# Kernel tuning notes

Hardware: AMD Instinct MI355X
Metric: run time of the kernel (lower is better)

## Reference

```python
import jax, jax.numpy as jnp
import numpy as np

B, N, D, H = 2, 2048, 1024, 16
DH = D // H            # 64
PH = 3 * DH            # 192 per-head proj dim (module quirk: 3*Dh per head)
P = H * PH             # 3072 total projection width


def setup_inputs() -> dict:
    key = jax.random.key(0)
    ks = jax.random.split(key, 8)
    s = 0.02
    return {
        "input": jax.random.normal(ks[0], (B, N, D), dtype=jnp.float32),
        "q_w": jax.random.normal(ks[1], (D, P), dtype=jnp.float32) * s,
        "q_b": jnp.zeros((P,), dtype=jnp.float32),
        "k_w": jax.random.normal(ks[2], (D, P), dtype=jnp.float32) * s,
        "k_b": jnp.zeros((P,), dtype=jnp.float32),
        "v_w": jax.random.normal(ks[3], (D, P), dtype=jnp.float32) * s,
        "v_b": jnp.zeros((P,), dtype=jnp.float32),
        "o_w": jax.random.normal(ks[4], (P, D), dtype=jnp.float32) * s,
        "o_b": jnp.zeros((D,), dtype=jnp.float32),
    }


def reference(input, q_w, q_b, k_w, k_b, v_w, v_b, o_w, o_b):
    def heads(y):  # [B,N,H*PH] -> [B,H,N,PH]
        return y.reshape(B, N, H, PH).transpose(0, 2, 1, 3)

    q_mat = heads(input @ q_w + q_b)
    # faithful to source: v_mat uses the 'k' projection, k_mat uses the 'v' projection
    v_mat = heads(input @ k_w + k_b)
    k_mat = heads(input @ v_w + v_b)

    scale = 1.0 / jnp.sqrt(jnp.float32(DH * H))  # sqrt(dim), per source
    scores = jnp.einsum('bhnd,bhmd->bhnm', q_mat, k_mat) * scale
    weights = jax.nn.softmax(scores, axis=-1)
    inter = jnp.einsum('bhnm,bhmd->bhnd', weights, v_mat)
    inter = inter.transpose(0, 2, 1, 3).reshape(B, N, P)  # b n (h d)
    return inter @ o_w + o_b
```

## Files before the change

kernel.cpp:

```cpp
#include <hip/hip_runtime.h>
#include <cstdint>
#include <cstddef>

typedef __bf16 bf16;
typedef __attribute__((ext_vector_type(8))) __bf16 bf16x8;
typedef __attribute__((ext_vector_type(4))) __bf16 bf16x4;
typedef __attribute__((ext_vector_type(2))) __bf16 bf16x2;
typedef __attribute__((ext_vector_type(4))) float f32x4;

#define MFMA_16x16x32(a, b, c) __builtin_amdgcn_mfma_f32_16x16x32_bf16((a), (b), (c), 0, 0, 0)

__device__ __forceinline__ void gload_lds16(const void* g, void* l) {
  __builtin_amdgcn_global_load_lds((__attribute__((address_space(1))) void*)g,
                                   (__attribute__((address_space(3))) void*)l,
                                   16, 0, 0);
}

__global__ __launch_bounds__(256) void cvt_x_kernel(const float* __restrict__ in,
                                                    bf16* __restrict__ out) {
  int i = blockIdx.x * 256 + threadIdx.x;
  float4 v = ((const float4*)in)[i];
  bf16x4 o = {(bf16)v.x, (bf16)v.y, (bf16)v.z, (bf16)v.w};
  ((bf16x4*)out)[i] = o;
}

__global__ __launch_bounds__(256) void transpose_cvt_kernel(const float* __restrict__ in,
                                                            bf16* __restrict__ out,
                                                            int R, int C) {
  __shared__ float tile[32][33];
  int tiles_c = C >> 5;
  int br = (int)blockIdx.x / tiles_c, bc = (int)blockIdx.x % tiles_c;
  int r0 = br << 5, c0 = bc << 5;
  int tr = threadIdx.x >> 5, tc = threadIdx.x & 31;
#pragma unroll
  for (int i = 0; i < 4; i++)
    tile[tr + 8 * i][tc] = in[(size_t)(r0 + tr + 8 * i) * C + c0 + tc];
  __syncthreads();
#pragma unroll
  for (int i = 0; i < 4; i++) {
    int oc = tr + 8 * i;
    out[(size_t)(c0 + oc) * R + r0 + tc] = (bf16)tile[tc][oc];
  }
}

__global__ __launch_bounds__(512, 2) void gemm_fused_qkv(
    const bf16* __restrict__ A, const bf16* __restrict__ Bt,
    const float* __restrict__ q_b, const float* __restrict__ v_b,
    const float* __restrict__ k_b,
    bf16* __restrict__ Qm, bf16* __restrict__ Km, bf16* __restrict__ Vt) {
  constexpr int K = 1024, NT = 16;
  __shared__ __align__(16) bf16 sA[2][2][128 * 32];
  __shared__ __align__(16) bf16 sB[2][192 * 64];

  int bid = blockIdx.x;
  int xcd = bid & 7, j = bid >> 3;
  int bm = xcd * 4 + (j & 3), bn = j >> 2;
  int m0 = bm << 7, n0 = bn * 192;

  int tid = threadIdx.x, lane = tid & 63, w = tid >> 6;
  int wr = w >> 2, wc = w & 3;
  int l15 = lane & 15, lg = lane >> 4;

  int sra = lane >> 2, sca = lane & 3;
  const bf16* gA = A + (size_t)(m0 + w * 16 + sra) * K + ((sca ^ ((sra >> 1) & 3)) * 8);
  int srb = lane >> 3, scb = lane & 7;
  const bf16* gB = Bt + (size_t)(n0 + w * 24 + srb) * K + ((scb ^ srb) * 8);

#define STAGE_AB(BUF, T)                                                   \
  {                                                                        \
    _Pragma("unroll") for (int kh = 0; kh < 2; kh++)                       \
        gload_lds16(gA + (size_t)(T) * 64 + kh * 32, &sA[BUF][kh][w * 512]); \
    _Pragma("unroll") for (int ii = 0; ii < 3; ii++)                       \
        gload_lds16(gB + (size_t)(ii * 8) * K + (T) * 64,                  \
                    &sB[BUF][(w * 3 + ii) * 512]);                         \
  }
#define VMCNT(N) asm volatile("s_waitcnt vmcnt(" #N ")" ::: "memory")
#define LGK0                                           \
  {                                                    \
    asm volatile("s_waitcnt lgkmcnt(0)" ::: "memory"); \
    __builtin_amdgcn_sched_barrier(0);                 \
  }

  int slotA = lg ^ ((l15 >> 1) & 3);
  int aBase = wr * 2048 + l15 * 32 + slotA * 8;
  int bBase = (wc * 48 + l15) * 64;
  int sB0 = (lg ^ (l15 & 7)) * 8;
  int sB1 = ((4 + lg) ^ (l15 & 7)) * 8;

#define RD_A(BUF, KH)                                                      \
  _Pragma("unroll") for (int mf = 0; mf < 4; mf++)                         \
      a[mf] = *(const bf16x8*)&sA[BUF][KH][aBase + mf * 512];
#define RD_B(BUF, SLOT)                                                    \
  _Pragma("unroll") for (int nf = 0; nf < 3; nf++)                         \
      b[nf] = *(const bf16x8*)&sB[BUF][bBase + nf * 1024 + (SLOT)];
#define MFMA12                                                             \
  _Pragma("unroll") for (int mf = 0; mf < 4; mf++)                         \
      _Pragma("unroll") for (int nf = 0; nf < 3; nf++)                     \
          acc[mf][nf] = MFMA_16x16x32(a[mf], b[nf], acc[mf][nf]);

  f32x4 acc[4][3];
#pragma unroll
  for (int mf = 0; mf < 4; mf++)
#pragma unroll
    for (int nf = 0; nf < 3; nf++) acc[mf][nf] = (f32x4){0.f, 0.f, 0.f, 0.f};

  STAGE_AB(0, 0);

#pragma unroll 2
  for (int s = 0; s < NT; s++) {
    int buf = s & 1, nbuf = buf ^ 1;
    int nxt = (s + 1) & (NT - 1);
    bf16x8 a[4], b[3];

    STAGE_AB(nbuf, nxt);
    VMCNT(5);
    __builtin_amdgcn_s_barrier();

    RD_A(buf, 0);
    RD_B(buf, sB0);
    LGK0;
    __builtin_amdgcn_s_setprio(1);
    MFMA12;
    __builtin_amdgcn_s_setprio(0);

    RD_A(buf, 1);
    RD_B(buf, sB1);
    LGK0;
    __builtin_amdgcn_s_barrier();
    __builtin_amdgcn_s_setprio(1);
    MFMA12;
    __builtin_amdgcn_s_setprio(0);
  }

  int seg = bn >> 4;
  int segbn = bn & 15;
  const float* bias = seg == 0 ? q_b : (seg == 1 ? v_b : k_b);
  bf16* outQK = seg == 0 ? Qm : Km;
#pragma unroll
  for (int mf = 0; mf < 4; mf++) {
#pragma unroll
    for (int nf = 0; nf < 3; nf++) {
      int colL = segbn * 192 + wc * 48 + nf * 16 + l15;
      int row0 = m0 + wr * 64 + mf * 16 + lg * 4;
      float bv = bias[colL];
      if (seg < 2) {
#pragma unroll
        for (int r = 0; r < 4; r++)
          outQK[(size_t)(row0 + r) * 3072 + colL] = (bf16)(acc[mf][nf][r] + bv);
      } else {
        int hh = colL / 192, dd = colL % 192;
        int bi = row0 >> 11, nn = row0 & 2047;
        bf16x4 pk = {(bf16)(acc[mf][nf][0] + bv), (bf16)(acc[mf][nf][1] + bv),
                     (bf16)(acc[mf][nf][2] + bv), (bf16)(acc[mf][nf][3] + bv)};
        *(bf16x4*)(Vt + (((size_t)bi * 16 + hh) * 192 + dd) * 2048 + nn) = pk;
      }
    }
  }
#undef STAGE_AB
#undef VMCNT
#undef LGK0
#undef RD_A
#undef RD_B
#undef MFMA12
}

template <int EPI>
__global__ __launch_bounds__(256, 2) void gemm_bf16_kernel(const bf16* __restrict__ A,
                                                           const bf16* __restrict__ Bt,
                                                           const float* __restrict__ bias,
                                                           void* __restrict__ Cout,
                                                           int M, int N, int K) {
  __shared__ __align__(16) bf16 sA[128 * 64];
  __shared__ __align__(16) bf16 sB[128 * 64];
  int tiles_n = N >> 7;
  int bm = (int)blockIdx.x / tiles_n, bn = (int)blockIdx.x % tiles_n;
  int m0 = bm << 7, n0 = bn << 7;
  int tid = threadIdx.x, lane = tid & 63, w = tid >> 6;
  int wr = w >> 1, wc = w & 1;
  int l15 = lane & 15, lg = lane >> 4;
  int sr = lane >> 3, sc = lane & 7;

  f32x4 acc[4][4];
#pragma unroll
  for (int mf = 0; mf < 4; mf++)
#pragma unroll
    for (int nf = 0; nf < 4; nf++) acc[mf][nf] = (f32x4){0.f, 0.f, 0.f, 0.f};

  int nkt = K >> 6;
  for (int kt = 0; kt < nkt; kt++) {
    __syncthreads();
#pragma unroll
    for (int i = 0; i < 4; i++) {
      int iw = w * 4 + i;
      int row = iw * 8 + sr;
      gload_lds16(A + (size_t)(m0 + row) * K + kt * 64 + sc * 8, &sA[iw * 512]);
      gload_lds16(Bt + (size_t)(n0 + row) * K + kt * 64 + sc * 8, &sB[iw * 512]);
    }
    __syncthreads();
#pragma unroll
    for (int ks = 0; ks < 2; ks++) {
      bf16x8 af[4], bfr[4];
#pragma unroll
      for (int mf = 0; mf < 4; mf++)
        af[mf] = *(const bf16x8*)&sA[(wr * 64 + mf * 16 + l15) * 64 + ks * 32 + lg * 8];
#pragma unroll
      for (int nf = 0; nf < 4; nf++)
        bfr[nf] = *(const bf16x8*)&sB[(wc * 64 + nf * 16 + l15) * 64 + ks * 32 + lg * 8];
#pragma unroll
      for (int mf = 0; mf < 4; mf++)
#pragma unroll
        for (int nf = 0; nf < 4; nf++)
          acc[mf][nf] = MFMA_16x16x32(af[mf], bfr[nf], acc[mf][nf]);
    }
  }

#pragma unroll
  for (int mf = 0; mf < 4; mf++) {
#pragma unroll
    for (int nf = 0; nf < 4; nf++) {
      int col = n0 + wc * 64 + nf * 16 + l15;
      int row0 = m0 + wr * 64 + mf * 16 + lg * 4;
      float biasv = bias[col];
      float* out = (float*)Cout;
#pragma unroll
      for (int r = 0; r < 4; r++)
        out[(size_t)(row0 + r) * N + col] = acc[mf][nf][r] + biasv;
    }
  }
}

__global__ __launch_bounds__(512, 2) void attn_kernel(const bf16* __restrict__ Q,
                                                      const bf16* __restrict__ Km,
                                                      const bf16* __restrict__ Vt,
                                                      bf16* __restrict__ inter) {
  __shared__ __align__(16) bf16 sK[2][64 * 192];
  __shared__ __align__(16) bf16 sV[2][192 * 64];
  __shared__ __align__(16) bf16 sPT[8 * 2 * 16 * 72];

  int i = blockIdx.x;
  int j = i >> 3;
  int bh = (i & 7) * 4 + (j >> 3);
  int qt = j & 7;
  int b = bh >> 4, h = bh & 15;
  int tid = threadIdx.x, lane = tid & 63, w = tid >> 6;
  int l15 = lane & 15, lg = lane >> 4;
  int swz = l15 & 7;

  const bf16* Qh = Q + (size_t)b * 2048 * 3072 + (size_t)h * 192;
  const bf16* Kh = Km + (size_t)b * 2048 * 3072 + (size_t)h * 192;
  const bf16* Vh = Vt + (size_t)bh * 192 * 2048;

  int q0 = qt * 256 + w * 32;

  int kOff[3], vOff[3], ldsOff[3];
#pragma unroll
  for (int ii = 0; ii < 3; ii++) {
    int r = ii * 8 + w;
    int s = r * 64 + lane;
    int krow = s / 24, kc = s % 24;
    int kcs = (kc & 24) | ((kc & 7) ^ (krow & 7));
    kOff[ii] = krow * 3072 + kcs * 8;
    int vrow = s >> 3, vc = s & 7;
    int vcs = vc ^ (vrow & 7);
    vOff[ii] = vrow * 2048 + vcs * 8;
    ldsOff[ii] = r * 512;
  }

#define STAGE(BUF, KT)                                                      \
  {                                                                         \
    int kb = (KT) * 64;                                                     \
    _Pragma("unroll") for (int ii = 0; ii < 3; ii++) {                      \
      gload_lds16(Kh + (size_t)kb * 3072 + kOff[ii], &sK[BUF][ldsOff[ii]]); \
      gload_lds16(Vh + kb + vOff[ii], &sV[BUF][ldsOff[ii]]);                \
    }                                                                       \
  }

  STAGE(0, 0);

  bf16x8 aq[2][6];
#pragma unroll
  for (int rf = 0; rf < 2; rf++)
#pragma unroll
    for (int kc = 0; kc < 6; kc++)
      aq[rf][kc] = *(const bf16x8*)(Qh + (size_t)(q0 + rf * 16 + l15) * 3072 + kc * 32 + lg * 8);

  f32x4 o[2][12];
#pragma unroll
  for (int rf = 0; rf < 2; rf++)
#pragma unroll
    for (int df = 0; df < 12; df++) o[rf][df] = (f32x4){0.f, 0.f, 0.f, 0.f};
  float mrow[2] = {-1e30f, -1e30f};
  float lrow[2] = {0.f, 0.f};

  const float scl2 = 0.03125f * 1.44269504f;

  bf16* myPT0 = &sPT[((w * 2 + 0) * 16 + l15) * 72];
  bf16* myPT1 = &sPT[((w * 2 + 1) * 16 + l15) * 72];

  __syncthreads();

  for (int kt = 0; kt < 32; kt++) {
    const bf16* kbuf = sK[kt & 1];
    const bf16* vbuf = sV[kt & 1];
    if (kt < 31) STAGE((kt & 1) ^ 1, kt + 1);

    f32x4 st[4][2];
#pragma unroll
    for (int kf = 0; kf < 4; kf++)
#pragma unroll
      for (int rf = 0; rf < 2; rf++) st[kf][rf] = (f32x4){0.f, 0.f, 0.f, 0.f};
    __builtin_amdgcn_s_setprio(1);
#pragma unroll
    for (int kc = 0; kc < 6; kc++) {
      int g = kc * 4 + lg;
      int cc = (g & 24) | ((g & 7) ^ swz);
#pragma unroll
      for (int kf = 0; kf < 4; kf++) {
        bf16x8 bk = *(const bf16x8*)&kbuf[(kf * 16 + l15) * 192 + cc * 8];
        st[kf][0] = MFMA_16x16x32(bk, aq[0][kc], st[kf][0]);
        st[kf][1] = MFMA_16x16x32(bk, aq[1][kc], st[kf][1]);
      }
    }
    __builtin_amdgcn_s_setprio(0);

#pragma unroll
    for (int rf = 0; rf < 2; rf++) {
      bf16* myPT = rf ? myPT1 : myPT0;
      float mk[4];
#pragma unroll
      for (int kf = 0; kf < 4; kf++)
        mk[kf] = fmaxf(fmaxf(st[kf][rf][0], st[kf][rf][1]),
                       fmaxf(st[kf][rf][2], st[kf][rf][3]));
      float pmx = fmaxf(fmaxf(mk[0], mk[1]), fmaxf(mk[2], mk[3]));
      pmx = fmaxf(pmx, __shfl_xor(pmx, 16));
      pmx = fmaxf(pmx, __shfl_xor(pmx, 32));
      float pms = pmx * scl2;

      float mn = mrow[rf];
      if (!__all(pms - mn <= 11.0f)) {
        mn = fmaxf(mn, pms);
        float corr = exp2f(mrow[rf] - mn);
        mrow[rf] = mn;
        lrow[rf] *= corr;
#pragma unroll
        for (int df = 0; df < 12; df++) o[rf][df] *= corr;
      }

      float skf[4];
#pragma unroll
      for (int kf = 0; kf < 4; kf++) {
        float e0 = exp2f(fmaf(st[kf][rf][0], scl2, -mn));
        float e1 = exp2f(fmaf(st[kf][rf][1], scl2, -mn));
        float e2 = exp2f(fmaf(st[kf][rf][2], scl2, -mn));
        float e3 = exp2f(fmaf(st[kf][rf][3], scl2, -mn));
        skf[kf] = (e0 + e1) + (e2 + e3);
        bf16x4 pk4 = {(bf16)e0, (bf16)e1, (bf16)e2, (bf16)e3};
        *(bf16x4*)&myPT[kf * 16 + 4 * lg] = pk4;
      }
      float rs = (skf[0] + skf[1]) + (skf[2] + skf[3]);
      rs += __shfl_xor(rs, 16);
      rs += __shfl_xor(rs, 32);
      lrow[rf] += rs;
    }

    bf16x8 pf[2][2];
#pragma unroll
    for (int rf = 0; rf < 2; rf++) {
      bf16* myPT = rf ? myPT1 : myPT0;
#pragma unroll
      for (int ks = 0; ks < 2; ks++)
        pf[rf][ks] = *(const bf16x8*)&myPT[ks * 32 + lg * 8];
    }

    __builtin_amdgcn_s_setprio(1);
#pragma unroll
    for (int ks = 0; ks < 2; ks++) {
      int cv = (ks * 4 + lg) ^ swz;
#pragma unroll
      for (int df = 0; df < 12; df++) {
        bf16x8 av = *(const bf16x8*)&vbuf[(df * 16 + l15) * 64 + cv * 8];
        o[0][df] = MFMA_16x16x32(av, pf[0][ks], o[0][df]);
        o[1][df] = MFMA_16x16x32(av, pf[1][ks], o[1][df]);
      }
    }
    __builtin_amdgcn_s_setprio(0);

    __syncthreads();
  }

#pragma unroll
  for (int rf = 0; rf < 2; rf++) {
    float inv = 1.0f / lrow[rf];
    size_t token = (size_t)b * 2048 + q0 + rf * 16 + l15;
    bf16* outp = inter + token * 3072 + h * 192 + lg * 4;
#pragma unroll
    for (int df = 0; df < 12; df++) {
      bf16x4 pk = {(bf16)(o[rf][df][0] * inv), (bf16)(o[rf][df][1] * inv),
                   (bf16)(o[rf][df][2] * inv), (bf16)(o[rf][df][3] * inv)};
      *(bf16x4*)(outp + df * 16) = pk;
    }
  }
#undef STAGE
}

extern "C" void kernel_launch(void* const* d_in, const int* in_sizes, int n_in,
                              void* d_out, int out_size, void* d_ws, size_t ws_size,
                              hipStream_t stream) {
  const float* X = (const float*)d_in[0];
  const float* q_w = (const float*)d_in[1];
  const float* q_b = (const float*)d_in[2];
  const float* k_w = (const float*)d_in[3];
  const float* k_b = (const float*)d_in[4];
  const float* v_w = (const float*)d_in[5];
  const float* v_b = (const float*)d_in[6];
  const float* o_w = (const float*)d_in[7];
  const float* o_b = (const float*)d_in[8];

  char* ws = (char*)d_ws;
  bf16* Xb  = (bf16*)(ws);
  bf16* Wqt = (bf16*)(ws + 8388608);
  bf16* Wvt = (bf16*)(ws + 14680064);
  bf16* Wkt = (bf16*)(ws + 20971520);
  bf16* Wot = (bf16*)(ws + 27262976);
  bf16* Qm  = (bf16*)(ws + 33554432);
  bf16* Km  = (bf16*)(ws + 58720256);
  bf16* Vtw = (bf16*)(ws + 83886080);
  bf16* Im  = (bf16*)(ws + 109051904);

  cvt_x_kernel<<<4096, 256, 0, stream>>>(X, Xb);
  transpose_cvt_kernel<<<3072, 256, 0, stream>>>(q_w, Wqt, 1024, 3072);
  transpose_cvt_kernel<<<3072, 256, 0, stream>>>(v_w, Wvt, 1024, 3072);
  transpose_cvt_kernel<<<3072, 256, 0, stream>>>(k_w, Wkt, 1024, 3072);
  transpose_cvt_kernel<<<3072, 256, 0, stream>>>(o_w, Wot, 3072, 1024);

  gemm_fused_qkv<<<1536, 512, 0, stream>>>(Xb, Wqt, q_b, v_b, k_b, Qm, Km, Vtw);

  attn_kernel<<<256, 512, 0, stream>>>(Qm, Km, Vtw, Im);

  gemm_bf16_kernel<2><<<256, 256, 0, stream>>>(Im, Wot, o_b, d_out, 4096, 1024, 3072);
}
```

Before: 304.8 us.

## Pipeline output-projection GEMM with double buffering and merge weight transposes

Replaces the simple synchronous output-projection GEMM with a specialized kernel that uses 128x64 tiles, double-buffered LDS staging with swizzled layout, vmcnt-based waits, priority hints and XCD-aware block mapping. It launches twice as many blocks to fill the GPU better. The three QKV weight transpose launches are merged into one kernel writing contiguously. The aim is to overlap global loads with MFMA work and to cut launch overhead, at the cost of more complex sync that relies on the VMCNT/LGK0 macros defined earlier.

```diff
diff --git a/kernel.cpp b/kernel.cpp
--- a/kernel.cpp
+++ b/kernel.cpp
@@ -40,6 +40,29 @@
   for (int i = 0; i < 4; i++) {
     int oc = tr + 8 * i;
     out[(size_t)(c0 + oc) * R + r0 + tc] = (bf16)tile[tc][oc];
+  }
+}
+
+__global__ __launch_bounds__(256) void transpose_cvt3_kernel(const float* __restrict__ q_w,
+                                                             const float* __restrict__ v_w,
+                                                             const float* __restrict__ k_w,
+                                                             bf16* __restrict__ out) {
+  __shared__ float tile[32][33];
+  int widx = (int)blockIdx.x / 3072;
+  int blk = (int)blockIdx.x % 3072;
+  const float* in = widx == 0 ? q_w : (widx == 1 ? v_w : k_w);
+  bf16* o = out + (size_t)widx * 3072 * 1024;
+  int br = blk / 96, bc = blk % 96;
+  int r0 = br << 5, c0 = bc << 5;
+  int tr = threadIdx.x >> 5, tc = threadIdx.x & 31;
+#pragma unroll
+  for (int i = 0; i < 4; i++)
+    tile[tr + 8 * i][tc] = in[(size_t)(r0 + tr + 8 * i) * 3072 + c0 + tc];
+  __syncthreads();
+#pragma unroll
+  for (int i = 0; i < 4; i++) {
+    int oc = tr + 8 * i;
+    o[(size_t)(c0 + oc) * 1024 + r0 + tc] = (bf16)tile[tc][oc];
   }
 }
 
@@ -157,76 +180,108 @@
     }
   }
 #undef STAGE_AB
-#undef VMCNT
-#undef LGK0
 #undef RD_A
 #undef RD_B
 #undef MFMA12
 }
 
-template <int EPI>
-__global__ __launch_bounds__(256, 2) void gemm_bf16_kernel(const bf16* __restrict__ A,
-                                                           const bf16* __restrict__ Bt,
-                                                           const float* __restrict__ bias,
-                                                           void* __restrict__ Cout,
-                                                           int M, int N, int K) {
-  __shared__ __align__(16) bf16 sA[128 * 64];
-  __shared__ __align__(16) bf16 sB[128 * 64];
-  int tiles_n = N >> 7;
-  int bm = (int)blockIdx.x / tiles_n, bn = (int)blockIdx.x % tiles_n;
-  int m0 = bm << 7, n0 = bn << 7;
+__global__ __launch_bounds__(256, 3) void gemm_oproj(const bf16* __restrict__ A,
+                                                     const bf16* __restrict__ Bt,
+                                                     const float* __restrict__ bias,
+                                                     float* __restrict__ out) {
+  constexpr int K = 3072, NT = 48;
+  __shared__ __align__(16) bf16 sA[2][2][128 * 32];
+  __shared__ __align__(16) bf16 sB[2][2][64 * 32];
+
+  int bid = blockIdx.x;
+  int xcd = bid & 7, j = bid >> 3;
+  int bm = xcd * 4 + (j & 3), bn = j >> 2;
+  int m0 = bm << 7, n0 = bn << 6;
+
   int tid = threadIdx.x, lane = tid & 63, w = tid >> 6;
   int wr = w >> 1, wc = w & 1;
   int l15 = lane & 15, lg = lane >> 4;
-  int sr = lane >> 3, sc = lane & 7;
-
-  f32x4 acc[4][4];
+
+  int sra = lane >> 2, sca = lane & 3;
+  int swzS = (sca ^ ((sra >> 1) & 3)) * 8;
+  const bf16* gA = A + (size_t)(m0 + w * 32 + sra) * K + swzS;
+  const bf16* gB = Bt + (size_t)(n0 + w * 16 + sra) * K + swzS;
+
+#define O_STAGE(BUF, T)                                                     \
+  {                                                                         \
+    _Pragma("unroll") for (int kh = 0; kh < 2; kh++) {                      \
+      _Pragma("unroll") for (int ii = 0; ii < 2; ii++)                      \
+          gload_lds16(gA + (size_t)(ii * 16) * K + (T) * 64 + kh * 32,      \
+                      &sA[BUF][kh][(w * 32 + ii * 16) * 32]);               \
+      gload_lds16(gB + (size_t)(T) * 64 + kh * 32, &sB[BUF][kh][w * 512]);  \
+    }                                                                       \
+  }
+
+  int slotA = lg ^ ((l15 >> 1) & 3);
+  int aBase = (wr * 64 + l15) * 32 + slotA * 8;
+  int bBase = (wc * 32 + l15) * 32 + slotA * 8;
+
+#define O_RD(BUF, KH)                                                      \
+  {                                                                        \
+    _Pragma("unroll") for (int mf = 0; mf < 4; mf++)                       \
+        a[mf] = *(const bf16x8*)&sA[BUF][KH][aBase + mf * 512];             \
+    _Pragma("unroll") for (int nf = 0; nf < 2; nf++)                       \
+        b[nf] = *(const bf16x8*)&sB[BUF][KH][bBase + nf * 512];             \
+  }
+#define O_MFMA8                                                            \
+  _Pragma("unroll") for (int mf = 0; mf < 4; mf++)                         \
+      _Pragma("unroll") for (int nf = 0; nf < 2; nf++)                     \
+          acc[mf][nf] = MFMA_16x16x32(a[mf], b[nf], acc[mf][nf]);
+
+  f32x4 acc[4][2];
 #pragma unroll
   for (int mf = 0; mf < 4; mf++)
 #pragma unroll
-    for (int nf = 0; nf < 4; nf++) acc[mf][nf] = (f32x4){0.f, 0.f, 0.f, 0.f};
-
-  int nkt = K >> 6;
-  for (int kt = 0; kt < nkt; kt++) {
-    __syncthreads();
-#pragma unroll
-    for (int i = 0; i < 4; i++) {
-      int iw = w * 4 + i;
-      int row = iw * 8 + sr;
-      gload_lds16(A + (size_t)(m0 + row) * K + kt * 64 + sc * 8, &sA[iw * 512]);
-      gload_lds16(Bt + (size_t)(n0 + row) * K + kt * 64 + sc * 8, &sB[iw * 512]);
-    }
-    __syncthreads();
-#pragma unroll
-    for (int ks = 0; ks < 2; ks++) {
-      bf16x8 af[4], bfr[4];
-#pragma unroll
-      for (int mf = 0; mf < 4; mf++)
-        af[mf] = *(const bf16x8*)&sA[(wr * 64 + mf * 16 + l15) * 64 + ks * 32 + lg * 8];
-#pragma unroll
-      for (int nf = 0; nf < 4; nf++)
-        bfr[nf] = *(const bf16x8*)&sB[(wc * 64 + nf * 16 + l15) * 64 + ks * 32 + lg * 8];
-#pragma unroll
-      for (int mf = 0; mf < 4; mf++)
-#pragma unroll
-        for (int nf = 0; nf < 4; nf++)
-          acc[mf][nf] = MFMA_16x16x32(af[mf], bfr[nf], acc[mf][nf]);
-    }
+    for (int nf = 0; nf < 2; nf++) acc[mf][nf] = (f32x4){0.f, 0.f, 0.f, 0.f};
+
+  O_STAGE(0, 0);
+
+#pragma unroll 2
+  for (int s = 0; s < NT; s++) {
+    int buf = s & 1, nbuf = buf ^ 1;
+    int nxt = s + 1 < NT ? s + 1 : 0;
+    bf16x8 a[4], b[2];
+
+    O_STAGE(nbuf, nxt);
+    VMCNT(6);
+    __builtin_amdgcn_s_barrier();
+
+    O_RD(buf, 0);
+    LGK0;
+    __builtin_amdgcn_s_setprio(1);
+    O_MFMA8;
+    __builtin_amdgcn_s_setprio(0);
+
+    O_RD(buf, 1);
+    LGK0;
+    __builtin_amdgcn_s_barrier();
+    __builtin_amdgcn_s_setprio(1);
+    O_MFMA8;
+    __builtin_amdgcn_s_setprio(0);
   }
 
 #pragma unroll
   for (int mf = 0; mf < 4; mf++) {
 #pragma unroll
-    for (int nf = 0; nf < 4; nf++) {
-      int col = n0 + wc * 64 + nf * 16 + l15;
+    for (int nf = 0; nf < 2; nf++) {
+      int col = n0 + wc * 32 + nf * 16 + l15;
       int row0 = m0 + wr * 64 + mf * 16 + lg * 4;
-      float biasv = bias[col];
-      float* out = (float*)Cout;
+      float bv = bias[col];
 #pragma unroll
       for (int r = 0; r < 4; r++)
-        out[(size_t)(row0 + r) * N + col] = acc[mf][nf][r] + biasv;
-    }
-  }
+        out[(size_t)(row0 + r) * 1024 + col] = acc[mf][nf][r] + bv;
+    }
+  }
+#undef O_STAGE
+#undef O_RD
+#undef O_MFMA8
+#undef VMCNT
+#undef LGK0
 }
 
 __global__ __launch_bounds__(512, 2) void attn_kernel(const bf16* __restrict__ Q,
@@ -419,8 +474,6 @@
   char* ws = (char*)d_ws;
   bf16* Xb  = (bf16*)(ws);
   bf16* Wqt = (bf16*)(ws + 8388608);
-  bf16* Wvt = (bf16*)(ws + 14680064);
-  bf16* Wkt = (bf16*)(ws + 20971520);
   bf16* Wot = (bf16*)(ws + 27262976);
   bf16* Qm  = (bf16*)(ws + 33554432);
   bf16* Km  = (bf16*)(ws + 58720256);
@@ -428,14 +481,12 @@
   bf16* Im  = (bf16*)(ws + 109051904);
 
   cvt_x_kernel<<<4096, 256, 0, stream>>>(X, Xb);
-  transpose_cvt_kernel<<<3072, 256, 0, stream>>>(q_w, Wqt, 1024, 3072);
-  transpose_cvt_kernel<<<3072, 256, 0, stream>>>(v_w, Wvt, 1024, 3072);
-  transpose_cvt_kernel<<<3072, 256, 0, stream>>>(k_w, Wkt, 1024, 3072);
+  transpose_cvt3_kernel<<<9216, 256, 0, stream>>>(q_w, v_w, k_w, Wqt);
   transpose_cvt_kernel<<<3072, 256, 0, stream>>>(o_w, Wot, 3072, 1024);
 
   gemm_fused_qkv<<<1536, 512, 0, stream>>>(Xb, Wqt, q_b, v_b, k_b, Qm, Km, Vtw);
 
   attn_kernel<<<256, 512, 0, stream>>>(Qm, Km, Vtw, Im);
 
-  gemm_bf16_kernel<2><<<256, 256, 0, stream>>>(Im, Wot, o_b, d_out, 4096, 1024, 3072);
-}
+  gemm_oproj<<<512, 256, 0, stream>>>(Im, Wot, o_b, (float*)d_out);
+}
```

Measured after the change: 277.5 us. 8.9% less time.
